# Kernel tuning notes

Hardware: AMD Instinct MI355X
Metric: run time of the kernel (lower is better)

Reference implementation:

```python
import math
import jax, jax.numpy as jnp
import numpy as np

V, BS, L, C, H, B, T = 50257, 2048, 4, 768, 12, 2, 2048
D = C // H


def layer_norm(x, g, b, eps=1e-5):
    m = x.mean(-1, keepdims=True)
    v = ((x - m) ** 2).mean(-1, keepdims=True)
    return (x - m) / jnp.sqrt(v + eps) * g + b


def setup_inputs() -> dict:
    key = jax.random.key(0)
    ks = jax.random.split(key, 10)
    s = 0.02
    inp = {}
    inp["idx"] = jax.random.randint(ks[0], (B, T), 0, V)
    inp["tok_emb"] = jax.random.normal(ks[1], (V, C), jnp.float32) * s
    inp["pos_emb"] = jax.random.normal(ks[2], (BS, C), jnp.float32) * s
    inp["ln1_g"] = jnp.ones((L, C)); inp["ln1_b"] = jnp.zeros((L, C))
    inp["qkv_w"] = jax.random.normal(ks[3], (L, C, 3 * C), jnp.float32) * s
    inp["qkv_b"] = jnp.zeros((L, 3 * C))
    inp["aproj_w"] = jax.random.normal(ks[4], (L, C, C), jnp.float32) * s
    inp["aproj_b"] = jnp.zeros((L, C))
    inp["ln2_g"] = jnp.ones((L, C)); inp["ln2_b"] = jnp.zeros((L, C))
    inp["fc_w"] = jax.random.normal(ks[5], (L, C, 4 * C), jnp.float32) * s
    inp["fc_b"] = jnp.zeros((L, 4 * C))
    inp["mproj_w"] = jax.random.normal(ks[6], (L, 4 * C, C), jnp.float32) * s
    inp["mproj_b"] = jnp.zeros((L, C))
    inp["lnf_g"] = jnp.ones((C,)); inp["lnf_b"] = jnp.zeros((C,))
    inp["head_w"] = jax.random.normal(ks[7], (C, V), jnp.float32) * s
    return inp


def reference(idx, tok_emb, pos_emb, ln1_g, ln1_b, qkv_w, qkv_b, aproj_w, aproj_b,
              ln2_g, ln2_b, fc_w, fc_b, mproj_w, mproj_b, lnf_g, lnf_b, head_w):
    b, t = idx.shape
    x = tok_emb[idx] + pos_emb[:t][None]  # [B,T,C]; dropout p=0 -> identity
    mask = jnp.tril(jnp.ones((t, t), bool))  # causal
    neg_inf = jnp.finfo(x.dtype).min
    n_layer = qkv_w.shape[0]
    for l in range(n_layer):
        h = layer_norm(x, ln1_g[l], ln1_b[l])
        qkv = h @ qkv_w[l] + qkv_b[l]  # [B,T,3C]
        q, k, v = jnp.split(qkv, 3, axis=-1)
        q = q.reshape(b, t, H, D).transpose(0, 2, 1, 3)  # [B,H,T,D]
        k = k.reshape(b, t, H, D).transpose(0, 2, 1, 3)
        v = v.reshape(b, t, H, D).transpose(0, 2, 1, 3)
        att = jnp.einsum('bhqd,bhkd->bhqk', q, k) / math.sqrt(D)
        att = jnp.where(mask, att, neg_inf)
        att = jax.nn.softmax(att, axis=-1)
        y = jnp.einsum('bhqk,bhkd->bhqd', att, v)
        y = y.transpose(0, 2, 1, 3).reshape(b, t, C)
        x = x + (y @ aproj_w[l] + aproj_b[l])
        h2 = layer_norm(x, ln2_g[l], ln2_b[l])
        hid = jax.nn.gelu(h2 @ fc_w[l] + fc_b[l], approximate=False)  # exact erf GELU (torch default)
        x = x + (hid @ mproj_w[l] + mproj_b[l])
    x = layer_norm(x, lnf_g, lnf_b)
    logits = x @ head_w  # [B,T,V]
    return logits
```

## Files before the change

kernel.cpp:

```cpp
#include <hip/hip_runtime.h>
#include <cstdint>
#include <cstddef>

#define Tn 2048
#define Bn 2
#define Hn 12
#define Cn 768
#define Ln 4
#define Vn 50257

typedef unsigned short ushort_t;
typedef __attribute__((ext_vector_type(8))) __bf16 bf16x8;
typedef __attribute__((ext_vector_type(8))) unsigned short u16x8;
typedef __attribute__((ext_vector_type(4))) float f32x4;

static constexpr size_t QKV_ELEMS = (size_t)Bn * Hn * Tn * 64;

__device__ inline unsigned short f2bf(float f) {
  unsigned int u = __float_as_uint(f);
  unsigned int r = (u + 0x7fffu + ((u >> 16) & 1u)) >> 16;
  return (unsigned short)r;
}

__device__ inline f32x4 zero4() { f32x4 z; z[0]=0.f; z[1]=0.f; z[2]=0.f; z[3]=0.f; return z; }

__device__ inline void gload_lds16(const ushort_t* g, ushort_t* l) {
  __builtin_amdgcn_global_load_lds(
      (const __attribute__((address_space(1))) void*)g,
      (__attribute__((address_space(3))) void*)l, 16, 0, 0);
}

__device__ inline int swz_lin() {
  int nbm = gridDim.x;
  int lin = blockIdx.y * nbm + blockIdx.x;
  int nwg = nbm * gridDim.y;
  int q = nwg >> 3, r = nwg & 7, x = lin & 7, p = lin >> 3;
  return (x < r ? x * (q + 1) : r * (q + 1) + (x - r) * q) + p;
}

__global__ __launch_bounds__(256) void embed_kernel(const int* __restrict__ idx,
    const float* __restrict__ tok, const float* __restrict__ pos, float* __restrict__ x) {
  int row = blockIdx.x;
  int t = row & (Tn - 1);
  int token = idx[row];
  const float* tr = tok + (size_t)token * Cn;
  const float* pr = pos + (size_t)t * Cn;
  float* xr = x + (size_t)row * Cn;
  for (int c = threadIdx.x; c < Cn; c += 256) xr[c] = tr[c] + pr[c];
}

__global__ __launch_bounds__(256) void ln_kernel(const float* __restrict__ x,
    const float* __restrict__ gam, const float* __restrict__ bet, ushort_t* __restrict__ out) {
  int row = blockIdx.x;
  const float* xr = x + (size_t)row * Cn;
  float v[3]; float s = 0.f, s2 = 0.f;
  #pragma unroll
  for (int e = 0; e < 3; ++e) { float t = xr[threadIdx.x + e*256]; v[e] = t; s += t; s2 += t*t; }
  #pragma unroll
  for (int off = 32; off >= 1; off >>= 1) { s += __shfl_xor(s, off); s2 += __shfl_xor(s2, off); }
  __shared__ float red[8];
  int w = threadIdx.x >> 6;
  if ((threadIdx.x & 63) == 0) { red[w] = s; red[4 + w] = s2; }
  __syncthreads();
  s  = red[0] + red[1] + red[2] + red[3];
  s2 = red[4] + red[5] + red[6] + red[7];
  float mean = s * (1.f / Cn);
  float var  = s2 * (1.f / Cn) - mean * mean;
  float rstd = rsqrtf(var + 1e-5f);
  ushort_t* orow = out + (size_t)row * Cn;
  #pragma unroll
  for (int e = 0; e < 3; ++e) {
    int c = threadIdx.x + e*256;
    orow[c] = f2bf((v[e] - mean) * rstd * gam[c] + bet[c]);
  }
}

__global__ __launch_bounds__(256) void tcvt_kernel(const float* __restrict__ in,
    ushort_t* __restrict__ out, int K, int N, int Npad) {
  __shared__ float tile[32][33];
  int n0 = blockIdx.x * 32, k0 = blockIdx.y * 32;
  int tx = threadIdx.x, ty = threadIdx.y;
  #pragma unroll
  for (int r = 0; r < 4; ++r) {
    int k = k0 + ty + 8*r;
    int n = n0 + tx;
    tile[ty + 8*r][tx] = (n < N) ? in[(size_t)k * N + n] : 0.f;
  }
  __syncthreads();
  #pragma unroll
  for (int r = 0; r < 4; ++r) {
    int n = n0 + ty + 8*r;
    out[(size_t)n * K + k0 + tx] = f2bf(tile[tx][ty + 8*r]);
  }
}

__global__ __launch_bounds__(256) void vtrans_kernel(const ushort_t* __restrict__ vin,
                                                     ushort_t* __restrict__ vout) {
  __shared__ ushort_t tile[64][65];
  int t0 = blockIdx.x * 64;
  size_t bh = blockIdx.y;
  const ushort_t* src = vin + (bh * Tn + t0) * 64;
  int row = threadIdx.x >> 2, c0 = (threadIdx.x & 3) * 16;
  u16x8 a = *(const u16x8*)&src[(size_t)row * 64 + c0];
  u16x8 b = *(const u16x8*)&src[(size_t)row * 64 + c0 + 8];
  #pragma unroll
  for (int j = 0; j < 8; ++j) { tile[row][c0 + j] = a[j]; tile[row][c0 + 8 + j] = b[j]; }
  __syncthreads();
  int d = threadIdx.x >> 2, tq = (threadIdx.x & 3) * 16;
  u16x8 o0, o1;
  #pragma unroll
  for (int j = 0; j < 8; ++j) { o0[j] = tile[tq + j][d]; o1[j] = tile[tq + 8 + j][d]; }
  ushort_t* dst = vout + (bh * 64 + d) * Tn + t0 + tq;
  *(u16x8*)&dst[0] = o0;
  *(u16x8*)&dst[8] = o1;
}

template<int MODE, int TM>
__global__ __launch_bounds__(256) void gemm_kernel(
    const ushort_t* __restrict__ A, const ushort_t* __restrict__ Bt,
    const float* __restrict__ bias, void* __restrict__ outp,
    const float* __restrict__ res, int M, int N, int K) {
  constexpr int MI = TM / 32;
  constexpr int ABUF = TM * 32;
  __shared__ ushort_t As[2 * ABUF];
  __shared__ ushort_t Bs[2 * 4096];
  const int t = threadIdx.x;

  int bm, bn;
  {
    int seq = swz_lin();
    const int G = 8;
    int NBN = gridDim.y;
    int gsz = G * NBN;
    int grp = seq / gsz;
    int t2 = seq - grp * gsz;
    bn = t2 / G;
    bm = grp * G + (t2 - bn * G);
  }
  const int w = t >> 6, l = t & 63, lo = l & 15, g = l >> 4;
  const int wm = w >> 1, wn = w & 1;

  f32x4 acc[MI][4];
  #pragma unroll
  for (int i = 0; i < MI; ++i)
    #pragma unroll
    for (int j = 0; j < 4; ++j) acc[i][j] = zero4();

  const int srow = t >> 2;
  const int scol = (t & 3) * 8;
  const ushort_t* gA = A  + (size_t)(bm * TM  + srow) * K + scol;
  const ushort_t* gB = Bt + (size_t)(bn * 128 + srow) * K + scol;
  ushort_t* lA = As + w * 512;
  ushort_t* lB = Bs + w * 512;

  auto stage = [&](int buf, int k0) {
    gload_lds16(gA + k0, lA + buf * ABUF);
    if (TM == 128) gload_lds16(gA + (size_t)64 * K + k0, lA + buf * ABUF + 2048);
    gload_lds16(gB + k0, lB + buf * 4096);
    gload_lds16(gB + (size_t)64 * K + k0, lB + buf * 4096 + 2048);
  };
  auto compute = [&](int buf) {
    const ushort_t* as = As + buf * ABUF;
    const ushort_t* bs = Bs + buf * 4096;
    bf16x8 af[MI], bfr[4];
    #pragma unroll
    for (int mi = 0; mi < MI; ++mi)
      af[mi] = *(const bf16x8*)&as[(size_t)(wm*(TM/2) + mi*16 + lo) * 32 + g*8];
    #pragma unroll
    for (int ni = 0; ni < 4; ++ni)
      bfr[ni] = *(const bf16x8*)&bs[(size_t)(wn*64 + ni*16 + lo) * 32 + g*8];
    #pragma unroll
    for (int mi = 0; mi < MI; ++mi)
      #pragma unroll
      for (int ni = 0; ni < 4; ++ni)
        acc[mi][ni] = __builtin_amdgcn_mfma_f32_16x16x32_bf16(af[mi], bfr[ni], acc[mi][ni], 0, 0, 0);
  };

  const int NK = K >> 5;
  stage(0, 0);
  __syncthreads();
  for (int kk = 0; kk < NK - 1; ++kk) {
    stage((kk + 1) & 1, (kk + 1) << 5);
    compute(kk & 1);
    __syncthreads();
  }
  compute((NK - 1) & 1);

  #pragma unroll
  for (int mi = 0; mi < MI; ++mi) {
    #pragma unroll
    for (int ni = 0; ni < 4; ++ni) {
      int colg = bn*128 + wn*64 + ni*16 + lo;
      if (colg < N) {
        float bv = bias ? bias[colg] : 0.f;
        #pragma unroll
        for (int i = 0; i < 4; ++i) {
          int rowg = bm*TM + wm*(TM/2) + mi*16 + 4*g + i;
          float vv = acc[mi][ni][i] + bv;
          if (MODE == 0) {
            ((float*)outp)[(size_t)rowg * N + colg] = vv;
          } else if (MODE == 1) {
            size_t off = (size_t)rowg * N + colg;
            ((float*)outp)[off] = res[off] + vv;
          } else if (MODE == 2) {
            float ge = 0.5f * vv * (1.f + erff(vv * 0.70710678118f));
            ((ushort_t*)outp)[(size_t)rowg * N + colg] = f2bf(ge);
          } else {
            int which = colg / Cn;
            int rem = colg - which * Cn;
            int h = rem >> 6, d = rem & 63;
            int b = rowg >> 11, tt = rowg & (Tn - 1);
            ushort_t* qb = (ushort_t*)outp;
            size_t bh = (size_t)(b * Hn + h);
            size_t off = (bh * Tn + tt) * 64 + d;
            if (which == 0)      qb[off] = f2bf(vv * 0.125f);
            else if (which == 1) qb[QKV_ELEMS + off] = f2bf(vv);
            else                 qb[3*QKV_ELEMS + off] = f2bf(vv);
          }
        }
      }
    }
  }
}

__global__ __launch_bounds__(64) void attn_kernel(const ushort_t* __restrict__ qkvh,
                                                  ushort_t* __restrict__ y) {
  const int l = threadIdx.x;
  const int lo = l & 15, g = l >> 4;
  int nl = swz_lin();
  const int qt = nl & 127;
  const int bh = nl >> 7;
  const int b = bh / Hn, h = bh % Hn;
  const int q0 = qt * 16;
  const ushort_t* Qp = qkvh + (size_t)bh * Tn * 64;
  const ushort_t* Kp = qkvh + QKV_ELEMS + (size_t)bh * Tn * 64;
  const ushort_t* Vt = qkvh + 2*QKV_ELEMS + (size_t)bh * 64 * Tn;

  bf16x8 qf[2];
  #pragma unroll
  for (int ch = 0; ch < 2; ++ch)
    qf[ch] = *(const bf16x8*)&Qp[(size_t)(q0 + lo) * 64 + ch*32 + g*8];

  f32x4 of[4];
  #pragma unroll
  for (int ch = 0; ch < 4; ++ch) of[ch] = zero4();
  float m = -1e30f, lsum = 0.f;
  const int nkv = q0 + 16;
  const bool ghi = (g >= 2);
  const int lg2 = (g & 1) * 32;

  for (int kv0 = 0; kv0 < nkv; kv0 += 32) {
    bf16x8 vf[4];
    #pragma unroll
    for (int ch = 0; ch < 4; ++ch)
      vf[ch] = *(const bf16x8*)&Vt[(size_t)(ch*16 + lo) * Tn + kv0 + g*8];

    float s8[8];
    #pragma unroll
    for (int sub = 0; sub < 2; ++sub) {
      int kvb = kv0 + 16*sub;
      bf16x8 kf[2];
      #pragma unroll
      for (int ch = 0; ch < 2; ++ch)
        kf[ch] = *(const bf16x8*)&Kp[(size_t)(kvb + lo) * 64 + ch*32 + g*8];
      f32x4 st = zero4();
      st = __builtin_amdgcn_mfma_f32_16x16x32_bf16(kf[0], qf[0], st, 0, 0, 0);
      st = __builtin_amdgcn_mfma_f32_16x16x32_bf16(kf[1], qf[1], st, 0, 0, 0);
      #pragma unroll
      for (int i = 0; i < 4; ++i) {
        int kvi = kvb + 4*g + i;
        s8[sub*4 + i] = (kvi <= q0 + lo) ? st[i] : -1e30f;
      }
    }
    float tmax = s8[0];
    #pragma unroll
    for (int j = 1; j < 8; ++j) tmax = fmaxf(tmax, s8[j]);
    tmax = fmaxf(tmax, __shfl_xor(tmax, 16));
    tmax = fmaxf(tmax, __shfl_xor(tmax, 32));
    float newm = fmaxf(m, tmax);
    float resc = __expf(m - newm);
    float p8[8]; float psum = 0.f;
    #pragma unroll
    for (int j = 0; j < 8; ++j) { p8[j] = __expf(s8[j] - newm); psum += p8[j]; }
    psum += __shfl_xor(psum, 16);
    psum += __shfl_xor(psum, 32);
    lsum = lsum * resc + psum;
    m = newm;
    #pragma unroll
    for (int i = 0; i < 4; ++i) {
      float rs = __shfl(resc, 4*g + i);
      of[0][i] *= rs; of[1][i] *= rs; of[2][i] *= rs; of[3][i] *= rs;
    }
    unsigned int q4[4];
    #pragma unroll
    for (int c = 0; c < 4; ++c)
      q4[c] = (unsigned int)f2bf(p8[2*c]) | ((unsigned int)f2bf(p8[2*c+1]) << 16);
    union { unsigned int wv[4]; bf16x8 v; } pu;
    #pragma unroll
    for (int j = 0; j < 4; ++j) {
      int srcLane = lo + lg2 + ((j >> 1) << 4);
      unsigned int lo_w = (unsigned int)__shfl((int)q4[j & 1], srcLane);
      unsigned int hi_w = (unsigned int)__shfl((int)q4[2 + (j & 1)], srcLane);
      pu.wv[j] = ghi ? hi_w : lo_w;
    }
    #pragma unroll
    for (int ch = 0; ch < 4; ++ch)
      of[ch] = __builtin_amdgcn_mfma_f32_16x16x32_bf16(pu.v, vf[ch], of[ch], 0, 0, 0);
  }

  #pragma unroll
  for (int i = 0; i < 4; ++i) {
    float li = 1.f / __shfl(lsum, 4*g + i);
    of[0][i] *= li; of[1][i] *= li; of[2][i] *= li; of[3][i] *= li;
  }
  ushort_t* yb = y + ((size_t)b*Tn + q0) * Cn + h*64;
  #pragma unroll
  for (int ch = 0; ch < 4; ++ch)
    #pragma unroll
    for (int i = 0; i < 4; ++i)
      yb[(size_t)(4*g + i) * Cn + ch*16 + lo] = f2bf(of[ch][i]);
}

extern "C" void kernel_launch(void* const* d_in, const int* in_sizes, int n_in,
                              void* d_out, int out_size, void* d_ws, size_t ws_size,
                              hipStream_t stream) {
  const int*   idx     = (const int*)d_in[0];
  const float* tok_emb = (const float*)d_in[1];
  const float* pos_emb = (const float*)d_in[2];
  const float* ln1_g   = (const float*)d_in[3];
  const float* ln1_b   = (const float*)d_in[4];
  const float* qkv_w   = (const float*)d_in[5];
  const float* qkv_b   = (const float*)d_in[6];
  const float* aproj_w = (const float*)d_in[7];
  const float* aproj_b = (const float*)d_in[8];
  const float* ln2_g   = (const float*)d_in[9];
  const float* ln2_b   = (const float*)d_in[10];
  const float* fc_w    = (const float*)d_in[11];
  const float* fc_b    = (const float*)d_in[12];
  const float* mproj_w = (const float*)d_in[13];
  const float* mproj_b = (const float*)d_in[14];
  const float* lnf_g   = (const float*)d_in[15];
  const float* lnf_b   = (const float*)d_in[16];
  const float* head_w  = (const float*)d_in[17];
  float* out = (float*)d_out;

  char* ws = (char*)d_ws;
  float*    x    = (float*)(ws);
  ushort_t* hA   = (ushort_t*)(ws + 12582912);
  ushort_t* hB   = (ushort_t*)(ws + 18874368);
  ushort_t* qkvh = (ushort_t*)(ws + 44040192);
  ushort_t* wT   = (ushort_t*)(ws + 69206016);

  const int M = Bn * Tn;
  dim3 tb(32, 8);

  embed_kernel<<<M, 256, 0, stream>>>(idx, tok_emb, pos_emb, x);
  for (int l = 0; l < Ln; ++l) {
    ln_kernel<<<M, 256, 0, stream>>>(x, ln1_g + l*Cn, ln1_b + l*Cn, hA);
    tcvt_kernel<<<dim3(2304/32, 768/32), tb, 0, stream>>>(qkv_w + (size_t)l*Cn*3*Cn, wT, 768, 2304, 2304);
    gemm_kernel<3,128><<<dim3(M/128, 2304/128), 256, 0, stream>>>(hA, wT, qkv_b + (size_t)l*3*Cn, qkvh, nullptr, M, 2304, 768);
    vtrans_kernel<<<dim3(Tn/64, Bn*Hn), 256, 0, stream>>>(qkvh + 3*QKV_ELEMS, qkvh + 2*QKV_ELEMS);
    attn_kernel<<<dim3(128, Bn*Hn), 64, 0, stream>>>(qkvh, hA);
    tcvt_kernel<<<dim3(768/32, 768/32), tb, 0, stream>>>(aproj_w + (size_t)l*Cn*Cn, wT, 768, 768, 768);
    gemm_kernel<1,64><<<dim3(M/64, 768/128), 256, 0, stream>>>(hA, wT, aproj_b + (size_t)l*Cn, x, x, M, 768, 768);
    ln_kernel<<<M, 256, 0, stream>>>(x, ln2_g + l*Cn, ln2_b + l*Cn, hA);
    tcvt_kernel<<<dim3(3072/32, 768/32), tb, 0, stream>>>(fc_w + (size_t)l*Cn*4*Cn, wT, 768, 3072, 3072);
    gemm_kernel<2,128><<<dim3(M/128, 3072/128), 256, 0, stream>>>(hA, wT, fc_b + (size_t)l*4*Cn, hB, nullptr, M, 3072, 768);
    tcvt_kernel<<<dim3(768/32, 3072/32), tb, 0, stream>>>(mproj_w + (size_t)l*4*Cn*Cn, wT, 3072, 768, 768);
    gemm_kernel<1,64><<<dim3(M/64, 768/128), 256, 0, stream>>>(hB, wT, mproj_b + (size_t)l*Cn, x, x, M, 768, 3072);
  }
  ln_kernel<<<M, 256, 0, stream>>>(x, lnf_g, lnf_b, hA);
  tcvt_kernel<<<dim3(50304/32, 768/32), tb, 0, stream>>>(head_w, wT, 768, Vn, 50304);
  gemm_kernel<0,128><<<dim3(M/128, 50304/128), 256, 0, stream>>>(hA, wT, nullptr, out, nullptr, M, Vn, 768);
}
```

Before: 1.852 ms.

## Add 256x256-tile GEMM with triple-buffered LDS pipeline for large GEMMs

Adds a new 512-thread GEMM kernel with 256x256 output tiles, a three-stage LDS buffer ring, explicit vmcnt waits and raised MFMA priority. It is used for the QKV, FC and LM-head GEMMs; the older kernel is kept only for the residual-add projections. Larger tiles raise arithmetic intensity and reduce global traffic per FLOP. In exchange each block needs far more LDS and registers, and the head weight padding grows to 50432 columns.

```diff
diff --git a/kernel.cpp b/kernel.cpp
--- a/kernel.cpp
+++ b/kernel.cpp
@@ -115,93 +115,101 @@
   *(u16x8*)&dst[8] = o1;
 }
 
-template<int MODE, int TM>
-__global__ __launch_bounds__(256) void gemm_kernel(
+template<int MODE>
+__global__ __launch_bounds__(512, 2) void gemm256_kernel(
     const ushort_t* __restrict__ A, const ushort_t* __restrict__ Bt,
     const float* __restrict__ bias, void* __restrict__ outp,
-    const float* __restrict__ res, int M, int N, int K) {
-  constexpr int MI = TM / 32;
-  constexpr int ABUF = TM * 32;
-  __shared__ ushort_t As[2 * ABUF];
-  __shared__ ushort_t Bs[2 * 4096];
+    int M, int N, int K) {
+  __shared__ ushort_t lds[3 * 16384];
   const int t = threadIdx.x;
+  const int w = t >> 6, l = t & 63, lo = l & 15, g = l >> 4;
+  const int wm = w >> 2, wn = w & 3;
 
   int bm, bn;
   {
     int seq = swz_lin();
-    const int G = 8;
-    int NBN = gridDim.y;
-    int gsz = G * NBN;
+    int gsz = 8 * gridDim.y;
     int grp = seq / gsz;
     int t2 = seq - grp * gsz;
-    bn = t2 / G;
-    bm = grp * G + (t2 - bn * G);
-  }
-  const int w = t >> 6, l = t & 63, lo = l & 15, g = l >> 4;
-  const int wm = w >> 1, wn = w & 1;
-
-  f32x4 acc[MI][4];
-  #pragma unroll
-  for (int i = 0; i < MI; ++i)
+    bn = t2 >> 3;
+    bm = grp * 8 + (t2 & 7);
+  }
+
+  const ushort_t* gAb = A  + (size_t)bm * 256 * K;
+  const ushort_t* gBb = Bt + (size_t)bn * 256 * K;
+
+  f32x4 acc[8][4];
+  #pragma unroll
+  for (int i = 0; i < 8; ++i)
     #pragma unroll
     for (int j = 0; j < 4; ++j) acc[i][j] = zero4();
 
-  const int srow = t >> 2;
-  const int scol = (t & 3) * 8;
-  const ushort_t* gA = A  + (size_t)(bm * TM  + srow) * K + scol;
-  const ushort_t* gB = Bt + (size_t)(bn * 128 + srow) * K + scol;
-  ushort_t* lA = As + w * 512;
-  ushort_t* lB = Bs + w * 512;
-
-  auto stage = [&](int buf, int k0) {
-    gload_lds16(gA + k0, lA + buf * ABUF);
-    if (TM == 128) gload_lds16(gA + (size_t)64 * K + k0, lA + buf * ABUF + 2048);
-    gload_lds16(gB + k0, lB + buf * 4096);
-    gload_lds16(gB + (size_t)64 * K + k0, lB + buf * 4096 + 2048);
+  auto stage = [&](int kt, int buf) {
+    int k0 = kt << 5;
+    #pragma unroll
+    for (int j = 0; j < 2; ++j) {
+      int ch = j * 512 + t;
+      gload_lds16(gAb + (size_t)(ch >> 2) * K + k0 + (ch & 3) * 8,
+                  &lds[buf * 16384 + j * 4096 + w * 512]);
+      gload_lds16(gBb + (size_t)(ch >> 2) * K + k0 + (ch & 3) * 8,
+                  &lds[buf * 16384 + 8192 + j * 4096 + w * 512]);
+    }
   };
   auto compute = [&](int buf) {
-    const ushort_t* as = As + buf * ABUF;
-    const ushort_t* bs = Bs + buf * 4096;
-    bf16x8 af[MI], bfr[4];
-    #pragma unroll
-    for (int mi = 0; mi < MI; ++mi)
-      af[mi] = *(const bf16x8*)&as[(size_t)(wm*(TM/2) + mi*16 + lo) * 32 + g*8];
+    const ushort_t* as = &lds[buf * 16384];
+    const ushort_t* bs = &lds[buf * 16384 + 8192];
+    bf16x8 af[8], bfr[4];
+    #pragma unroll
+    for (int mi = 0; mi < 8; ++mi)
+      af[mi] = *(const bf16x8*)&as[(wm*128 + mi*16 + lo) * 32 + g*8];
     #pragma unroll
     for (int ni = 0; ni < 4; ++ni)
-      bfr[ni] = *(const bf16x8*)&bs[(size_t)(wn*64 + ni*16 + lo) * 32 + g*8];
-    #pragma unroll
-    for (int mi = 0; mi < MI; ++mi)
+      bfr[ni] = *(const bf16x8*)&bs[(wn*64 + ni*16 + lo) * 32 + g*8];
+    __builtin_amdgcn_s_setprio(1);
+    #pragma unroll
+    for (int mi = 0; mi < 8; ++mi)
       #pragma unroll
       for (int ni = 0; ni < 4; ++ni)
         acc[mi][ni] = __builtin_amdgcn_mfma_f32_16x16x32_bf16(af[mi], bfr[ni], acc[mi][ni], 0, 0, 0);
+    __builtin_amdgcn_s_setprio(0);
   };
 
   const int NK = K >> 5;
-  stage(0, 0);
-  __syncthreads();
-  for (int kk = 0; kk < NK - 1; ++kk) {
-    stage((kk + 1) & 1, (kk + 1) << 5);
-    compute(kk & 1);
-    __syncthreads();
-  }
-  compute((NK - 1) & 1);
-
-  #pragma unroll
-  for (int mi = 0; mi < MI; ++mi) {
+  stage(0, 0); stage(1, 1); stage(2, 2);
+  asm volatile("s_waitcnt vmcnt(8)" ::: "memory");
+  __builtin_amdgcn_s_barrier();
+
+  int buf = 0;
+  #pragma unroll 1
+  for (int kt = 0; kt < NK; ++kt) {
+    compute(buf);
+    asm volatile("s_waitcnt lgkmcnt(0)" ::: "memory");
+    __builtin_amdgcn_s_barrier();
+    if (kt + 3 < NK) {
+      stage(kt + 3, buf);
+      asm volatile("s_waitcnt vmcnt(8)" ::: "memory");
+    } else if (kt + 2 < NK) {
+      asm volatile("s_waitcnt vmcnt(4)" ::: "memory");
+    } else {
+      asm volatile("s_waitcnt vmcnt(0)" ::: "memory");
+    }
+    __builtin_amdgcn_s_barrier();
+    buf = (buf == 2) ? 0 : buf + 1;
+  }
+
+  #pragma unroll
+  for (int mi = 0; mi < 8; ++mi) {
     #pragma unroll
     for (int ni = 0; ni < 4; ++ni) {
-      int colg = bn*128 + wn*64 + ni*16 + lo;
+      int colg = bn*256 + wn*64 + ni*16 + lo;
       if (colg < N) {
         float bv = bias ? bias[colg] : 0.f;
         #pragma unroll
         for (int i = 0; i < 4; ++i) {
-          int rowg = bm*TM + wm*(TM/2) + mi*16 + 4*g + i;
+          int rowg = bm*256 + wm*128 + mi*16 + 4*g + i;
           float vv = acc[mi][ni][i] + bv;
           if (MODE == 0) {
             ((float*)outp)[(size_t)rowg * N + colg] = vv;
-          } else if (MODE == 1) {
-            size_t off = (size_t)rowg * N + colg;
-            ((float*)outp)[off] = res[off] + vv;
           } else if (MODE == 2) {
             float ge = 0.5f * vv * (1.f + erff(vv * 0.70710678118f));
             ((ushort_t*)outp)[(size_t)rowg * N + colg] = f2bf(ge);
@@ -217,6 +225,95 @@
             else if (which == 1) qb[QKV_ELEMS + off] = f2bf(vv);
             else                 qb[3*QKV_ELEMS + off] = f2bf(vv);
           }
+        }
+      }
+    }
+  }
+}
+
+template<int MODE, int TM>
+__global__ __launch_bounds__(256) void gemm_kernel(
+    const ushort_t* __restrict__ A, const ushort_t* __restrict__ Bt,
+    const float* __restrict__ bias, void* __restrict__ outp,
+    const float* __restrict__ res, int M, int N, int K) {
+  constexpr int MI = TM / 32;
+  constexpr int ABUF = TM * 32;
+  __shared__ ushort_t As[2 * ABUF];
+  __shared__ ushort_t Bs[2 * 4096];
+  const int t = threadIdx.x;
+  int bm, bn;
+  {
+    int seq = swz_lin();
+    const int G = 8;
+    int NBN = gridDim.y;
+    int gsz = G * NBN;
+    int grp = seq / gsz;
+    int t2 = seq - grp * gsz;
+    bn = t2 / G;
+    bm = grp * G + (t2 - bn * G);
+  }
+  const int w = t >> 6, l = t & 63, lo = l & 15, g = l >> 4;
+  const int wm = w >> 1, wn = w & 1;
+
+  f32x4 acc[MI][4];
+  #pragma unroll
+  for (int i = 0; i < MI; ++i)
+    #pragma unroll
+    for (int j = 0; j < 4; ++j) acc[i][j] = zero4();
+
+  const int srow = t >> 2;
+  const int scol = (t & 3) * 8;
+  const ushort_t* gA = A  + (size_t)(bm * TM  + srow) * K + scol;
+  const ushort_t* gB = Bt + (size_t)(bn * 128 + srow) * K + scol;
+  ushort_t* lA = As + w * 512;
+  ushort_t* lB = Bs + w * 512;
+
+  auto stage = [&](int buf, int k0) {
+    gload_lds16(gA + k0, lA + buf * ABUF);
+    if (TM == 128) gload_lds16(gA + (size_t)64 * K + k0, lA + buf * ABUF + 2048);
+    gload_lds16(gB + k0, lB + buf * 4096);
+    gload_lds16(gB + (size_t)64 * K + k0, lB + buf * 4096 + 2048);
+  };
+  auto compute = [&](int buf) {
+    const ushort_t* as = As + buf * ABUF;
+    const ushort_t* bs = Bs + buf * 4096;
+    bf16x8 af[MI], bfr[4];
+    #pragma unroll
+    for (int mi = 0; mi < MI; ++mi)
+      af[mi] = *(const bf16x8*)&as[(size_t)(wm*(TM/2) + mi*16 + lo) * 32 + g*8];
+    #pragma unroll
+    for (int ni = 0; ni < 4; ++ni)
+      bfr[ni] = *(const bf16x8*)&bs[(size_t)(wn*64 + ni*16 + lo) * 32 + g*8];
+    #pragma unroll
+    for (int mi = 0; mi < MI; ++mi)
+      #pragma unroll
+      for (int ni = 0; ni < 4; ++ni)
+        acc[mi][ni] = __builtin_amdgcn_mfma_f32_16x16x32_bf16(af[mi], bfr[ni], acc[mi][ni], 0, 0, 0);
+  };
+
+  const int NK = K >> 5;
+  stage(0, 0);
+  __syncthreads();
+  for (int kk = 0; kk < NK - 1; ++kk) {
+    stage((kk + 1) & 1, (kk + 1) << 5);
+    compute(kk & 1);
+    __syncthreads();
+  }
+  compute((NK - 1) & 1);
+
+  #pragma unroll
+  for (int mi = 0; mi < MI; ++mi) {
+    #pragma unroll
+    for (int ni = 0; ni < 4; ++ni) {
+      int colg = bn*128 + wn*64 + ni*16 + lo;
+      if (colg < N) {
+        float bv = bias ? bias[colg] : 0.f;
+        #pragma unroll
+        for (int i = 0; i < 4; ++i) {
+          int rowg = bm*TM + wm*(TM/2) + mi*16 + 4*g + i;
+          size_t off = (size_t)rowg * N + colg;
+          float vv = acc[mi][ni][i] + bv;
+          ((float*)outp)[off] = res[off] + vv;
         }
       }
     }
@@ -358,18 +455,18 @@
   for (int l = 0; l < Ln; ++l) {
     ln_kernel<<<M, 256, 0, stream>>>(x, ln1_g + l*Cn, ln1_b + l*Cn, hA);
     tcvt_kernel<<<dim3(2304/32, 768/32), tb, 0, stream>>>(qkv_w + (size_t)l*Cn*3*Cn, wT, 768, 2304, 2304);
-    gemm_kernel<3,128><<<dim3(M/128, 2304/128), 256, 0, stream>>>(hA, wT, qkv_b + (size_t)l*3*Cn, qkvh, nullptr, M, 2304, 768);
+    gemm256_kernel<3><<<dim3(M/256, 2304/256), 512, 0, stream>>>(hA, wT, qkv_b + (size_t)l*3*Cn, qkvh, M, 2304, 768);
     vtrans_kernel<<<dim3(Tn/64, Bn*Hn), 256, 0, stream>>>(qkvh + 3*QKV_ELEMS, qkvh + 2*QKV_ELEMS);
     attn_kernel<<<dim3(128, Bn*Hn), 64, 0, stream>>>(qkvh, hA);
     tcvt_kernel<<<dim3(768/32, 768/32), tb, 0, stream>>>(aproj_w + (size_t)l*Cn*Cn, wT, 768, 768, 768);
     gemm_kernel<1,64><<<dim3(M/64, 768/128), 256, 0, stream>>>(hA, wT, aproj_b + (size_t)l*Cn, x, x, M, 768, 768);
     ln_kernel<<<M, 256, 0, stream>>>(x, ln2_g + l*Cn, ln2_b + l*Cn, hA);
     tcvt_kernel<<<dim3(3072/32, 768/32), tb, 0, stream>>>(fc_w + (size_t)l*Cn*4*Cn, wT, 768, 3072, 3072);
-    gemm_kernel<2,128><<<dim3(M/128, 3072/128), 256, 0, stream>>>(hA, wT, fc_b + (size_t)l*4*Cn, hB, nullptr, M, 3072, 768);
+    gemm256_kernel<2><<<dim3(M/256, 3072/256), 512, 0, stream>>>(hA, wT, fc_b + (size_t)l*4*Cn, hB, M, 3072, 768);
     tcvt_kernel<<<dim3(768/32, 3072/32), tb, 0, stream>>>(mproj_w + (size_t)l*4*Cn*Cn, wT, 3072, 768, 768);
     gemm_kernel<1,64><<<dim3(M/64, 768/128), 256, 0, stream>>>(hB, wT, mproj_b + (size_t)l*Cn, x, x, M, 768, 3072);
   }
   ln_kernel<<<M, 256, 0, stream>>>(x, lnf_g, lnf_b, hA);
-  tcvt_kernel<<<dim3(50304/32, 768/32), tb, 0, stream>>>(head_w, wT, 768, Vn, 50304);
-  gemm_kernel<0,128><<<dim3(M/128, 50304/128), 256, 0, stream>>>(hA, wT, nullptr, out, nullptr, M, Vn, 768);
-}
+  tcvt_kernel<<<dim3(50432/32, 768/32), tb, 0, stream>>>(head_w, wT, 768, Vn, 50432);
+  gemm256_kernel<0><<<dim3(M/256, 50432/256), 512, 0, stream>>>(hA, wT, nullptr, out, M, Vn, 768);
+}
```

After: 2.180 ms. 1.18x slower.
